# Kernel optimization log

Hardware: AMD Instinct MI355X
Metric: run time of the kernel (lower is better)

Reference implementation:

```python
import jax, jax.numpy as jnp
import numpy as np
from math import factorial

N_NODES = 50000
N_EDGES = 500000
NUM_BASIS = 10
HIDDEN = 64
MUL_OUT = 8  # irreps_out_per_basis = '8x0e + 8x1o + 8x2e'

# ---------- real Wigner-3j (Clebsch-Gordan in real SH basis) ----------

def _cg(j1, m1, j2, m2, j3, m3):
    # complex Clebsch-Gordan <j1 m1 j2 m2 | j3 m3> (Racah formula)
    if m1 + m2 != m3:
        return 0.0
    f = factorial
    pre = ((2*j3+1) * f(j1+j2-j3) * f(j1-j2+j3) * f(-j1+j2+j3) / f(j1+j2+j3+1)) ** 0.5
    pre *= (f(j1+m1)*f(j1-m1)*f(j2+m2)*f(j2-m2)*f(j3+m3)*f(j3-m3)) ** 0.5
    s = 0.0
    for k in range(max(0, j2-j3-m1, j1-j3+m2), min(j1+j2-j3, j1-m1, j2+m2) + 1):
        s += (-1)**k / (f(k)*f(j1+j2-j3-k)*f(j1-m1-k)*f(j2+m2-k)*f(j3-j2+m1+k)*f(j3-j1-m2+k))
    return pre * s

def _q(l):
    # complex -> real spherical-harmonic change of basis, m ordered -l..l
    Q = np.zeros((2*l+1, 2*l+1), dtype=complex)
    Q[l, l] = 1.0
    for m in range(1, l+1):
        Q[l+m, l+m] = (-1)**m / np.sqrt(2.0); Q[l+m, l-m] = 1.0/np.sqrt(2.0)
        Q[l-m, l-m] = 1j / np.sqrt(2.0);      Q[l-m, l+m] = -1j*(-1)**m/np.sqrt(2.0)
    return Q

def _w3j(l1, l2, l3):
    C = np.zeros((2*l1+1, 2*l2+1, 2*l3+1), dtype=complex)
    for a, m1 in enumerate(range(-l1, l1+1)):
        for b, m2 in enumerate(range(-l2, l2+1)):
            for c, m3 in enumerate(range(-l3, l3+1)):
                C[a, b, c] = _cg(l1, m1, l2, m2, l3, m3)
    R = np.einsum('ab,cd,ef,bdf->ace', _q(l1).conj(), _q(l2).conj(), _q(l3), C)
    if np.abs(R.imag).max() > np.abs(R.real).max():
        R = -1j * R
    R = np.real(R)
    return (R / np.linalg.norm(R)).astype(np.float32)

# allowed (l2, l3) paths for each input block l1 (parity-filtered to 0e/1o/2e output)
PATHS = {0: [(0, 0), (1, 1), (2, 2)],
         1: [(0, 1), (1, 0), (1, 2), (2, 1)],
         2: [(0, 2), (1, 1), (2, 0), (2, 2)]}
MUL1 = {0: 1, 1: 3, 2: 5}
W3J = {(l1, l2, l3): jnp.asarray(_w3j(l1, l2, l3))
       for l1, ps in PATHS.items() for (l2, l3) in ps}
FAN = {l1: {l3: sum(MUL1[l1] for (_, l3b) in PATHS[l1] if l3b == l3) for l3 in (0, 1, 2)}
       for l1 in (0, 1, 2)}
WNUMEL = {l1: len(PATHS[l1]) * MUL1[l1] * MUL_OUT for l1 in (0, 1, 2)}  # 24, 96, 160

# ---------- forward pieces ----------

def _sh(unit):
    # component-normalized real spherical harmonics, lmax=2, e3nn (y,z,x) order for l=1
    x, y, z = unit[:, 0], unit[:, 1], unit[:, 2]
    sh0 = jnp.ones_like(x)[:, None]
    sh1 = jnp.sqrt(3.0) * jnp.stack([y, z, x], axis=1)
    sh2 = jnp.stack([jnp.sqrt(15.0)*x*y, jnp.sqrt(15.0)*y*z,
                     jnp.sqrt(5.0)/2.0*(3.0*z*z - 1.0), jnp.sqrt(15.0)*x*z,
                     jnp.sqrt(15.0)/2.0*(x*x - y*y)], axis=1)
    return {0: sh0, 1: sh1, 2: sh2}

def _soft_one_hot(d, max_radius):
    # e3nn soft_one_hot_linspace, basis='smooth_finite', cutoff=True
    values = jnp.linspace(0.0, float(max_radius), NUM_BASIS + 2)[1:-1]
    step = float(max_radius) / (NUM_BASIS + 1)
    diff = (d[:, None] - values) / step
    def sus(t):
        return jnp.where(t > 0.0, jnp.exp(-1.0 / jnp.where(t > 0.0, t, 1.0)), 0.0)
    e = 1.14136 * np.exp(2.0) * sus(diff + 1.0) * sus(1.0 - diff)
    return e * np.sqrt(float(NUM_BASIS))

def _fc(x, w1, w2):
    # e3nn FullyConnectedNet: variance-preserving linear + normalized relu
    h = (x @ w1) / np.sqrt(float(w1.shape[0]))
    h = jax.nn.relu(h) * np.sqrt(2.0)
    return (h @ w2) / np.sqrt(float(w2.shape[0]))

def _tp(l1, x1, shs, w_flat):
    # FullyConnectedTensorProduct (uvw, shared_weights=False, component/element norm)
    # x1: [E, mul1, 2l1+1], w_flat: [E, WNUMEL[l1]]
    E = x1.shape[0]
    outs = {l3: jnp.zeros((E, MUL_OUT, 2*l3+1), x1.dtype) for l3 in (0, 1, 2)}
    off = 0
    for (l2, l3) in PATHS[l1]:
        n = MUL1[l1] * MUL_OUT
        w = w_flat[:, off:off+n].reshape(E, MUL1[l1], MUL_OUT)
        off += n
        pw = np.sqrt((2*l3 + 1) / float(FAN[l1][l3]))
        outs[l3] = outs[l3] + pw * jnp.einsum('eui,ej,ijk,euw->ewk',
                                              x1, shs[l2], W3J[(l1, l2, l3)], w)
    return jnp.concatenate([outs[l3].reshape(E, -1) for l3 in (0, 1, 2)], axis=1)

def _forward(x, edge_index, pos, max_radius, num_nodes, ws1, ws2, wp1, wp2, wd1, wd2):
    row, col = edge_index[0], edge_index[1]
    edge_vec = pos[row] - pos[col]                          # [E,3]
    d = jnp.sqrt(jnp.sum(edge_vec * edge_vec, axis=1) + 1e-12)
    shs = _sh(edge_vec / d[:, None])
    emb = _soft_one_hot(d, max_radius)                      # [E,NUM_BASIS]
    w_s = _fc(emb, ws1, ws2)
    w_p = _fc(emb, wp1, wp2)
    w_d = _fc(emb, wd1, wd2)
    f = x.reshape(-1, 9, 9, 2)
    fsum = f[..., 0] + f[..., 1]  # TP is linear in input 1: tp(a,w)+tp(b,w)=tp(a+b,w)
    out_s = _tp(0, fsum[:, 0:1, 0:1].reshape(-1, 1, 1)[row], shs, w_s)
    out_p = _tp(1, fsum[:, 1:4, 1:4].reshape(-1, 3, 3)[row], shs, w_p)
    out_d = _tp(2, fsum[:, 4:9, 4:9].reshape(-1, 5, 5)[row], shs, w_d)
    summand = jnp.concatenate([out_s, out_p, out_d], axis=1)  # [E,216]
    f_out = jax.ops.segment_sum(summand, col, num_segments=num_nodes)
    return f_out / np.sqrt(edge_index.shape[1] / float(num_nodes))


def setup_inputs() -> dict:
    key = jax.random.key(0)
    ks = jax.random.split(key, 10)
    x = jax.random.normal(ks[0], (N_NODES, 162), jnp.float32)
    pos = jax.random.normal(ks[1], (N_NODES, 3), jnp.float32) * 2.0
    row = jax.random.randint(ks[2], (N_EDGES,), 0, N_NODES)
    col = (row + jax.random.randint(ks[3], (N_EDGES,), 1, N_NODES)) % N_NODES  # no self-loops
    edge_index = jnp.stack([row, col]).astype(jnp.int32)
    return {
        'x': x, 'edge_index': edge_index, 'pos': pos,
        'max_radius': 5, 'num_nodes': N_NODES,
        'fc_s_w1': jax.random.normal(ks[4], (NUM_BASIS, HIDDEN), jnp.float32),
        'fc_s_w2': jax.random.normal(ks[5], (HIDDEN, WNUMEL[0]), jnp.float32),
        'fc_p_w1': jax.random.normal(ks[6], (NUM_BASIS, HIDDEN), jnp.float32),
        'fc_p_w2': jax.random.normal(ks[7], (HIDDEN, WNUMEL[1]), jnp.float32),
        'fc_d_w1': jax.random.normal(ks[8], (NUM_BASIS, HIDDEN), jnp.float32),
        'fc_d_w2': jax.random.normal(ks[9], (HIDDEN, WNUMEL[2]), jnp.float32),
    }


def reference(x, edge_index, pos, max_radius, num_nodes,
              fc_s_w1, fc_s_w2, fc_p_w1, fc_p_w2, fc_d_w1, fc_d_w2):
    return _forward(x, edge_index, pos, max_radius, num_nodes,
                    fc_s_w1, fc_s_w2, fc_p_w1, fc_p_w2, fc_d_w1, fc_d_w2)
```

## Files before the change

### kernel.cpp

```cpp
#include <hip/hip_runtime.h>

#define BLK 128
#define RSTR 76
#define W1OFF (35*512)

__device__ __forceinline__ double dfac(int n){
  const double T[8] = {1.0,1.0,2.0,6.0,24.0,120.0,720.0,5040.0};
  return T[n];
}

__device__ __forceinline__ double cgc(int j1,int m1,int j2,int m2,int j3,int m3){
  if (m1+m2 != m3) return 0.0;
  double pre = sqrt((double)(2*j3+1) * dfac(j1+j2-j3)*dfac(j1-j2+j3)*dfac(-j1+j2+j3)/dfac(j1+j2+j3+1));
  pre *= sqrt(dfac(j1+m1)*dfac(j1-m1)*dfac(j2+m2)*dfac(j2-m2)*dfac(j3+m3)*dfac(j3-m3));
  int kmin = 0; if (j2-j3-m1 > kmin) kmin = j2-j3-m1; if (j1-j3+m2 > kmin) kmin = j1-j3+m2;
  int kmax = j1+j2-j3; if (j1-m1 < kmax) kmax = j1-m1; if (j2+m2 < kmax) kmax = j2+m2;
  double s = 0.0;
  for (int k=kmin;k<=kmax;++k){
    double t = 1.0/(dfac(k)*dfac(j1+j2-j3-k)*dfac(j1-m1-k)*dfac(j2+m2-k)*dfac(j3-j2+m1+k)*dfac(j3-j1-m2+k));
    s += (k&1)? -t : t;
  }
  return pre*s;
}

__device__ __forceinline__ void qval(int l, int a, int b, double& qr, double& qi){
  qr = 0.0; qi = 0.0;
  int ma = a - l, mb = b - l;
  if (ma==0){ if (mb==0) qr = 1.0; return; }
  const double is2 = 0.7071067811865476;
  if (ma > 0){
    if (mb == ma)       qr = (ma&1)? -is2 : is2;
    else if (mb == -ma) qr = is2;
  } else {
    int m = -ma;
    if (mb == ma)       qi = is2;
    else if (mb == m)   qi = (m&1)? is2 : -is2;
  }
}

__global__ __launch_bounds__(384) void w3j_kernel(float* __restrict__ w3j){
  __shared__ double Rr[363], Ri[363];
  __shared__ double sInv[11];
  __shared__ int    sFlip[11];
  const int L1t[11] = {0,0,0,1,1,1,1,2,2,2,2};
  const int L2t[11] = {0,1,2,0,1,1,2,0,1,2,2};
  const int L3t[11] = {0,1,2,1,0,2,1,2,1,0,2};
  const int OFFt[12]= {0,1,10,35,44,53,98,143,168,213,238,363};

  int g = threadIdx.x;
  bool act = g < 363;
  int t = 0, l1=0, l2=0, l3=0;
  if (act){
    while (g >= OFFt[t+1]) t++;
    l1=L1t[t]; l2=L2t[t]; l3=L3t[t];
    int n2=2*l2+1, n3=2*l3+1;
    int local = g - OFFt[t];
    int e  = local % n3;
    int tm = local / n3;
    int c  = tm % n2;
    int a  = tm / n2;
    double sr=0.0, si=0.0;
    for (int b=0; b<2*l1+1; b++){
      double q1r,q1i; qval(l1,a,b,q1r,q1i); q1i = -q1i;
      if (q1r==0.0 && q1i==0.0) continue;
      for (int dd=0; dd<n2; dd++){
        double q2r,q2i; qval(l2,c,dd,q2r,q2i); q2i = -q2i;
        if (q2r==0.0 && q2i==0.0) continue;
        double pr = q1r*q2r - q1i*q2i;
        double pi = q1r*q2i + q1i*q2r;
        for (int f=0; f<n3; f++){
          double cg = cgc(l1,b-l1,l2,dd-l2,l3,f-l3);
          if (cg==0.0) continue;
          double q3r,q3i; qval(l3,e,f,q3r,q3i);
          sr += cg*(pr*q3r - pi*q3i);
          si += cg*(pr*q3i + pi*q3r);
        }
      }
    }
    Rr[g]=sr; Ri[g]=si;
  }
  __syncthreads();
  if (threadIdx.x < 11){
    int tt = threadIdx.x;
    int lo = OFFt[tt], hi = OFFt[tt+1];
    double mxr=0.0, mxi=0.0;
    for (int i=lo;i<hi;i++){
      double ar=fabs(Rr[i]), ai=fabs(Ri[i]);
      if (ar>mxr) mxr=ar;
      if (ai>mxi) mxi=ai;
    }
    int flip = (mxi > mxr) ? 1 : 0;
    double nrm=0.0;
    for (int i=lo;i<hi;i++){ double v = flip? Ri[i] : Rr[i]; nrm += v*v; }
    sInv[tt]  = 1.0/sqrt(nrm);
    sFlip[tt] = flip;
  }
  __syncthreads();
  if (act){
    double v = sFlip[t] ? Ri[g] : Rr[g];
    w3j[g] = (float)(v * sInv[t]);
  }
}

__global__ void pack_kernel(const float* __restrict__ x, float* __restrict__ xp, int tot){
  int i = blockIdx.x*256 + threadIdx.x;
  if (i >= tot) return;
  int n = i/35, j = i - n*35;
  int src;
  if (j == 0)       src = 0;
  else if (j < 10){ int r=j-1;  src = (1 + r/3)*9 + 1 + r%3; }
  else            { int r=j-10; src = (4 + r/5)*9 + 4 + r%5; }
  const float* b = x + (size_t)n*162 + src*2;
  xp[i] = b[0] + b[1];
}

__global__ void repack_kernel(const float* __restrict__ w2s, const float* __restrict__ w2p,
                              const float* __restrict__ w2d,
                              const float* __restrict__ w1s, const float* __restrict__ w1p,
                              const float* __restrict__ w1d, float* __restrict__ wr){
  int i = blockIdx.x*256 + threadIdx.x;
  int tot2 = 35*512;
  if (i < tot2){
    int blk = i >> 9;
    int idx = i & 511;
    int hc = idx >> 3, w = idx & 7;
    const float* src; int WN, cb, u;
    if (blk < 3){ src=w2s; WN=24; cb=blk*8; u=0; }
    else if (blk < 15){ int b=blk-3; int p=b/3; u=b-p*3; src=w2p; WN=96; const int cbs[4]={0,24,48,72}; cb=cbs[p]; }
    else { int b=blk-15; int p=b/5; u=b-p*5; src=w2d; WN=160; const int cbs[4]={0,40,80,120}; cb=cbs[p]; }
    wr[i] = src[hc*WN + cb + u*8 + w];
  } else if (i < tot2 + 3*640){
    int r = i - tot2;
    int c = r/640; int rem = r - c*640;
    int chunk = rem/40; int idx = rem - chunk*40;
    int b = idx>>2, j = idx&3;
    const float* src = (c==0)? w1s : (c==1)? w1p : w1d;
    wr[i] = src[b*64 + chunk*4 + j];
  }
}

__device__ __forceinline__ bool edge_ok(const float* __restrict__ pos, int row, int col, float mrf){
  float ax = pos[3*row+0]-pos[3*col+0];
  float ay = pos[3*row+1]-pos[3*col+1];
  float az = pos[3*row+2]-pos[3*col+2];
  float d  = sqrtf(fmaf(ax,ax, fmaf(ay,ay, fmaf(az,az, 1e-12f))));
  return d < mrf;
}

__global__ void hist_kernel(const int* __restrict__ ei, const float* __restrict__ pos,
                            const int* __restrict__ mrp, int* __restrict__ cnt, int E){
  int e = blockIdx.x*256 + threadIdx.x;
  if (e >= E) return;
  int row = ei[e], col = ei[E+e];
  if (edge_ok(pos,row,col,(float)mrp[0])) atomicAdd(&cnt[col], 1);
}

__device__ __forceinline__ int wscan(int v, int lane){
  #pragma unroll
  for (int s=1;s<64;s<<=1){
    int t = __shfl_up(v, s);
    if (lane >= s) v += t;
  }
  return v;
}

__global__ void scan_kernel(int* __restrict__ cnt, int* __restrict__ off, int N){
  __shared__ int wsum[16];
  __shared__ int srun;
  int t=threadIdx.x, lane=t&63, w=t>>6;
  if (t==0) srun=0;
  __syncthreads();
  for (int base=0; base<N; base+=1024){
    int v = (base+t<N) ? cnt[base+t] : 0;
    int incl = wscan(v, lane);
    if (lane==63) wsum[w]=incl;
    __syncthreads();
    int run = srun;
    int woff = 0;
    for (int i=0;i<w;i++) woff += wsum[i];
    int ex = run + woff + incl - v;
    if (base+t<N){ off[base+t]=ex; cnt[base+t]=ex; }
    __syncthreads();
    if (t==1023) srun = run + woff + incl;
    __syncthreads();
  }
  if (t==0) off[N]=srun;
}

__global__ void scatter_kernel(const int* __restrict__ ei, const float* __restrict__ pos,
                               const int* __restrict__ mrp, int* __restrict__ cursor,
                               int* __restrict__ csrR, int* __restrict__ csrC, int E){
  int e = blockIdx.x*256 + threadIdx.x;
  if (e >= E) return;
  int row = ei[e], col = ei[E+e];
  if (edge_ok(pos,row,col,(float)mrp[0])){
    int s = atomicAdd(&cursor[col], 1);
    csrR[s] = row;
    csrC[s] = col;
  }
}

__device__ __forceinline__ void compute_h(const float (&emb)[10], const float* __restrict__ w1r, float* hrow){
  const float RS10 = 0.31622776601683794f;
  #pragma unroll 2
  for (int i=0; i<16; ++i){
    const float* r = w1r + i*40;
    float a0=0.f,a1=0.f,a2=0.f,a3=0.f;
    #pragma unroll
    for (int b=0;b<10;b++){
      a0 = fmaf(emb[b], r[b*4+0], a0);
      a1 = fmaf(emb[b], r[b*4+1], a1);
      a2 = fmaf(emb[b], r[b*4+2], a2);
      a3 = fmaf(emb[b], r[b*4+3], a3);
    }
    float4 hv;
    hv.x = fmaxf(a0*RS10, 0.f);
    hv.y = fmaxf(a1*RS10, 0.f);
    hv.z = fmaxf(a2*RS10, 0.f);
    hv.w = fmaxf(a3*RS10, 0.f);
    *reinterpret_cast<float4*>(hrow+i*4) = hv;
  }
}

__device__ __forceinline__ void compute_h_raw(const float (&emb)[10], const float* __restrict__ w1, float* hrow){
  const float RS10 = 0.31622776601683794f;
  #pragma unroll 1
  for (int hh=0; hh<64; hh+=4){
    float a0=0.f,a1=0.f,a2=0.f,a3=0.f;
    #pragma unroll
    for (int b=0;b<10;b++){
      const float* r = w1 + b*64 + hh;
      a0 = fmaf(emb[b], r[0], a0);
      a1 = fmaf(emb[b], r[1], a1);
      a2 = fmaf(emb[b], r[2], a2);
      a3 = fmaf(emb[b], r[3], a3);
    }
    float4 hv;
    hv.x = fmaxf(a0*RS10, 0.f);
    hv.y = fmaxf(a1*RS10, 0.f);
    hv.z = fmaxf(a2*RS10, 0.f);
    hv.w = fmaxf(a3*RS10, 0.f);
    *reinterpret_cast<float4*>(hrow+hh) = hv;
  }
}

template<int L1, int L2, int L3, int W3JOFF>
__device__ __forceinline__ void calc_s(const float* __restrict__ w3j,
    const float (&x1)[2*L1+1], const float (&sh1)[3], const float (&sh2)[5],
    float CP, float (&s)[2*L3+1])
{
  constexpr int N1=2*L1+1, N2=2*L2+1, N3=2*L3+1;
  #pragma unroll
  for (int k=0;k<N3;k++) s[k]=0.f;
  #pragma unroll
  for (int i=0;i<N1;i++){
    #pragma unroll
    for (int j=0;j<N2;j++){
      float shv = (L2==0) ? 1.0f : ((L2==1) ? sh1[j] : sh2[j]);
      float c = x1[i]*shv;
      #pragma unroll
      for (int k=0;k<N3;k++)
        s[k] = fmaf(c, w3j[W3JOFF + (i*N2+j)*N3 + k], s[k]);
    }
  }
  #pragma unroll
  for (int k=0;k<N3;k++) s[k] *= CP;
}

template<int P>
__device__ __forceinline__ void wg_pass_r(const float* __restrict__ wr,
    const int (&blks)[P], const float* __restrict__ hrow, float (&wg)[P][8])
{
  #pragma unroll
  for (int p=0;p<P;p++)
    #pragma unroll
    for (int w=0;w<8;w++) wg[p][w]=0.f;
  #pragma unroll 4
  for (int hc=0;hc<64;hc+=4){
    float4 hv = *reinterpret_cast<const float4*>(hrow+hc);
    #pragma unroll
    for (int p=0;p<P;p++){
      const float* r0 = wr + blks[p]*512 + hc*8;
      #pragma unroll
      for (int w=0;w<8;w++){
        float t0 = fmaf(hv.x, r0[w],    wg[p][w]);
        t0       = fmaf(hv.y, r0[8+w],  t0);
        t0       = fmaf(hv.z, r0[16+w], t0);
        wg[p][w] = fmaf(hv.w, r0[24+w], t0);
      }
    }
  }
}

template<int P, int WN>
__device__ __forceinline__ void wg_pass(const float* __restrict__ w2,
    const int (&cb)[P], int u8, const float* __restrict__ hrow, float (&wg)[P][8])
{
  #pragma unroll
  for (int p=0;p<P;p++)
    #pragma unroll
    for (int w=0;w<8;w++) wg[p][w]=0.f;
  #pragma unroll 1
  for (int hc=0;hc<64;hc+=4){
    float4 hv = *reinterpret_cast<const float4*>(hrow+hc);
    #pragma unroll
    for (int p=0;p<P;p++){
      const float* r0 = w2 + cb[p] + u8 + hc*WN;
      #pragma unroll
      for (int w=0;w<8;w++){
        float t0 = fmaf(hv.x, r0[w],      wg[p][w]);
        t0       = fmaf(hv.y, r0[WN+w],   t0);
        t0       = fmaf(hv.z, r0[2*WN+w], t0);
        wg[p][w] = fmaf(hv.w, r0[3*WN+w], t0);
      }
    }
  }
}

template<int N3, int OUTB>
__device__ __forceinline__ void acc_o(const float (&wgp)[8], const float (&s)[N3], float (&o)[72]){
  #pragma unroll
  for (int w=0;w<8;w++){
    #pragma unroll
    for (int k=0;k<N3;k++)
      o[OUTB + w*N3 + k] = fmaf(wgp[w], s[k], o[OUTB + w*N3 + k]);
  }
}

template<bool PACKED>
__global__ __launch_bounds__(BLK) void edge_kernel_csr(
  const int* __restrict__ csrR, const int* __restrict__ csrC,
  const int* __restrict__ off, int N,
  const float* __restrict__ pos, const float* __restrict__ x, const float* __restrict__ xp,
  const float* __restrict__ w3j, const int* __restrict__ mrp,
  const float* __restrict__ wr,
  float* __restrict__ out, float rs)
{
  __shared__ __align__(16) float hb[BLK*RSTR];
  __shared__ int scol[BLK];
  __shared__ int lmeta[BLK];
  __shared__ int lcount;

  int tid = threadIdx.x;
  int blockBase = blockIdx.x*BLK;
  int Ev = off[N];
  if (blockBase >= Ev) return;
  int slot = blockBase + tid;
  bool valid = slot < Ev;
  int row = valid ? csrR[slot] : 0;
  int key = valid ? csrC[slot] : -1;
  int colIdx = valid ? key : 0;

  scol[tid] = key;
  if (tid==0) lcount = 0;
  __syncthreads();
  if (valid && (tid==0 || scol[tid-1]!=key)){
    int len=1;
    while (tid+len<BLK && scol[tid+len]==key) len++;
    int comp = (off[key] >= blockBase) && (off[key+1] <= blockBase+BLK);
    int idx = atomicAdd(&lcount, 1);
    lmeta[idx] = tid | (len<<8) | (comp<<31);
  }
  __syncthreads();
  int lc = lcount;

  float ax = pos[3*row+0]-pos[3*colIdx+0];
  float ay = pos[3*row+1]-pos[3*colIdx+1];
  float az = pos[3*row+2]-pos[3*colIdx+2];
  float d  = sqrtf(fmaf(ax,ax, fmaf(ay,ay, fmaf(az,az, 1e-12f))));
  float mrf = (float)mrp[0];
  float inv = 1.0f/d;
  float ux=ax*inv, uy=ay*inv, uz=az*inv;
  float sh1[3] = {1.7320508075688772f*uy, 1.7320508075688772f*uz, 1.7320508075688772f*ux};
  float sh2[5] = {3.872983346207417f*ux*uy, 3.872983346207417f*uy*uz,
                  1.118033988749895f*(3.f*uz*uz-1.f), 3.872983346207417f*ux*uz,
                  1.9364916731037085f*(ux*ux-uy*uy)};
  float emb[10];
  {
    float xs = d * (11.0f/mrf);
    float CE = 1.14136f * expf(2.0f) * sqrtf(10.0f);
    #pragma unroll
    for (int b=0;b<10;b++){
      float t1 = xs - (float)b;
      float t2 = (float)(b+2) - xs;
      float s1 = (t1>0.f)? expf(-1.0f/t1) : 0.f;
      float s2 = (t2>0.f)? expf(-1.0f/t2) : 0.f;
      emb[b] = CE*s1*s2;
    }
  }

  float* hrow = &hb[tid*RSTR];
  const float* xrow = PACKED ? (xp + (size_t)row*35) : (x + (size_t)row*162);
  const float* w1r = wr + W1OFF;

  auto flush_reduce = [&](const float (&o)[72], int PO){
    #pragma unroll
    for (int i=0;i<72;i+=4){
      float4 v; v.x=o[i]; v.y=o[i+1]; v.z=o[i+2]; v.w=o[i+3];
      *reinterpret_cast<float4*>(hrow+i) = v;
    }
    __syncthreads();
    int total = lc*72;
    for (int task = tid; task < total; task += BLK){
      int li = task/72;
      int el = task - li*72;
      int meta = lmeta[li];
      int s0  = meta & 255;
      int len = (meta>>8) & 255;
      int c   = scol[s0];
      float sum = 0.f;
      const float* p = &hb[s0*RSTR + el];
      for (int i=0;i<len;i++) sum += p[i*RSTR];
      float* dst = out + (size_t)c*216 + PO + el;
      if (meta < 0) *dst = sum;
      else unsafeAtomicAdd(dst, sum);
    }
    __syncthreads();
  };

  {
    compute_h(emb, w1r + 0, hrow);
    float o[72];
    #pragma unroll
    for (int i=0;i<72;i++) o[i]=0.f;
    float x1[1];
    x1[0] = PACKED ? xrow[0] : (xrow[0]+xrow[1]);
    float sA[1], sB[3], sC[5];
    calc_s<0,0,0,  0>(w3j,x1,sh1,sh2, 0.17677669529663687f*rs, sA);
    calc_s<0,1,1,  1>(w3j,x1,sh1,sh2, 0.30618621784789724f*rs, sB);
    calc_s<0,2,2, 10>(w3j,x1,sh1,sh2, 0.39528470752104744f*rs, sC);
    float wg[3][8];
    const int blks[3] = {0,1,2};
    wg_pass_r<3>(wr, blks, hrow, wg);
    acc_o<1, 0>(wg[0], sA, o);
    acc_o<3, 8>(wg[1], sB, o);
    acc_o<5,32>(wg[2], sC, o);
    flush_reduce(o, 0);
  }
  {
    compute_h(emb, w1r + 640, hrow);
    float o[72];
    #pragma unroll
    for (int i=0;i<72;i++) o[i]=0.f;
    #pragma unroll 1
    for (int u=0;u<3;++u){
      float x1[3];
      #pragma unroll
      for (int i=0;i<3;i++){
        int src = ((1+u)*9 + 1+i)*2;
        x1[i] = PACKED ? xrow[1+u*3+i] : (xrow[src]+xrow[src+1]);
      }
      float sA[3], sB[1], sC[5], sD[3];
      calc_s<1,0,1, 35>(w3j,x1,sh1,sh2, 0.125f*rs,               sA);
      calc_s<1,1,0, 44>(w3j,x1,sh1,sh2, 0.10206207261596577f*rs, sB);
      calc_s<1,1,2, 53>(w3j,x1,sh1,sh2, 0.22821773229381923f*rs, sC);
      calc_s<1,2,1, 98>(w3j,x1,sh1,sh2, 0.125f*rs,               sD);
      float wg[4][8];
      const int blks[4] = {3+u, 6+u, 9+u, 12+u};
      wg_pass_r<4>(wr, blks, hrow, wg);
      acc_o<3, 8>(wg[0], sA, o);
      acc_o<1, 0>(wg[1], sB, o);
      acc_o<5,32>(wg[2], sC, o);
      acc_o<3, 8>(wg[3], sD, o);
    }
    flush_reduce(o, 72);
  }
  {
    compute_h(emb, w1r + 1280, hrow);
    float o[72];
    #pragma unroll
    for (int i=0;i<72;i++) o[i]=0.f;
    #pragma unroll 1
    for (int u=0;u<5;++u){
      float x1[5];
      #pragma unroll
      for (int i=0;i<5;i++){
        int src = ((4+u)*9 + 4+i)*2;
        x1[i] = PACKED ? xrow[10+u*5+i] : (xrow[src]+xrow[src+1]);
      }
      float sA[5], sB[3], sC[1], sD[5];
      calc_s<2,0,2,143>(w3j,x1,sh1,sh2, 0.125f*rs,               sA);
      calc_s<2,1,1,168>(w3j,x1,sh1,sh2, 0.13693063937629152f*rs, sB);
      calc_s<2,2,0,213>(w3j,x1,sh1,sh2, 0.07905694150420948f*rs, sC);
      calc_s<2,2,2,238>(w3j,x1,sh1,sh2, 0.125f*rs,               sD);
      float wg[4][8];
      const int blks[4] = {15+u, 20+u, 25+u, 30+u};
      wg_pass_r<4>(wr, blks, hrow, wg);
      acc_o<5,32>(wg[0], sA, o);
      acc_o<3, 8>(wg[1], sB, o);
      acc_o<1, 0>(wg[2], sC, o);
      acc_o<5,32>(wg[3], sD, o);
    }
    flush_reduce(o, 144);
  }
}

__device__ __forceinline__ void flush72(const float (&o)[72], float* dst){
  #pragma unroll
  for (int i=0;i<72;i++) unsafeAtomicAdd(dst+i, o[i]);
}

__global__ __launch_bounds__(BLK) void edge_kernel_atomic(
  const int* __restrict__ ei, const float* __restrict__ pos,
  const float* __restrict__ x,
  const float* __restrict__ w3j, const int* __restrict__ mrp,
  const float* __restrict__ w1s, const float* __restrict__ w2s,
  const float* __restrict__ w1p, const float* __restrict__ w2p,
  const float* __restrict__ w1d, const float* __restrict__ w2d,
  float* __restrict__ out, int E, float rs)
{
  __shared__ __align__(16) float hbA[BLK*RSTR];
  int e = blockIdx.x*BLK + threadIdx.x;
  if (e >= E) return;
  int row = ei[e], col = ei[E+e];
  float ax = pos[3*row+0]-pos[3*col+0];
  float ay = pos[3*row+1]-pos[3*col+1];
  float az = pos[3*row+2]-pos[3*col+2];
  float d  = sqrtf(fmaf(ax,ax, fmaf(ay,ay, fmaf(az,az, 1e-12f))));
  float mrf = (float)mrp[0];
  if (d >= mrf) return;
  float inv = 1.0f/d;
  float ux=ax*inv, uy=ay*inv, uz=az*inv;
  float sh1[3] = {1.7320508075688772f*uy, 1.7320508075688772f*uz, 1.7320508075688772f*ux};
  float sh2[5] = {3.872983346207417f*ux*uy, 3.872983346207417f*uy*uz,
                  1.118033988749895f*(3.f*uz*uz-1.f), 3.872983346207417f*ux*uz,
                  1.9364916731037085f*(ux*ux-uy*uy)};
  float emb[10];
  {
    float xs = d * (11.0f/mrf);
    float CE = 1.14136f * expf(2.0f) * sqrtf(10.0f);
    #pragma unroll
    for (int b=0;b<10;b++){
      float t1 = xs - (float)b;
      float t2 = (float)(b+2) - xs;
      float s1 = (t1>0.f)? expf(-1.0f/t1) : 0.f;
      float s2 = (t2>0.f)? expf(-1.0f/t2) : 0.f;
      emb[b] = CE*s1*s2;
    }
  }
  float* hrow = &hbA[threadIdx.x*RSTR];
  const float* xrow = x + (size_t)row*162;
  float* obase = out + (size_t)col*216;
  {
    compute_h_raw(emb, w1s, hrow);
    float o[72];
    #pragma unroll
    for (int i=0;i<72;i++) o[i]=0.f;
    float x1[1] = { xrow[0]+xrow[1] };
    float sA[1], sB[3], sC[5];
    calc_s<0,0,0,  0>(w3j,x1,sh1,sh2, 0.17677669529663687f*rs, sA);
    calc_s<0,1,1,  1>(w3j,x1,sh1,sh2, 0.30618621784789724f*rs, sB);
    calc_s<0,2,2, 10>(w3j,x1,sh1,sh2, 0.39528470752104744f*rs, sC);
    float wg[3][8];
    const int cb[3] = {0,8,16};
    wg_pass<3,24>(w2s, cb, 0, hrow, wg);
    acc_o<1, 0>(wg[0], sA, o);
    acc_o<3, 8>(wg[1], sB, o);
    acc_o<5,32>(wg[2], sC, o);
    flush72(o, obase);
  }
  {
    compute_h_raw(emb, w1p, hrow);
    float o[72];
    #pragma unroll
    for (int i=0;i<72;i++) o[i]=0.f;
    #pragma unroll 1
    for (int u=0;u<3;++u){
      float x1[3];
      #pragma unroll
      for (int i=0;i<3;i++){ int src = ((1+u)*9 + 1+i)*2; x1[i] = xrow[src]+xrow[src+1]; }
      float sA[3], sB[1], sC[5], sD[3];
      calc_s<1,0,1, 35>(w3j,x1,sh1,sh2, 0.125f*rs,               sA);
      calc_s<1,1,0, 44>(w3j,x1,sh1,sh2, 0.10206207261596577f*rs, sB);
      calc_s<1,1,2, 53>(w3j,x1,sh1,sh2, 0.22821773229381923f*rs, sC);
      calc_s<1,2,1, 98>(w3j,x1,sh1,sh2, 0.125f*rs,               sD);
      float wg[4][8];
      const int cb[4] = {0,24,48,72};
      wg_pass<4,96>(w2p, cb, u*8, hrow, wg);
      acc_o<3, 8>(wg[0], sA, o);
      acc_o<1, 0>(wg[1], sB, o);
      acc_o<5,32>(wg[2], sC, o);
      acc_o<3, 8>(wg[3], sD, o);
    }
    flush72(o, obase + 72);
  }
  {
    compute_h_raw(emb, w1d, hrow);
    float o[72];
    #pragma unroll
    for (int i=0;i<72;i++) o[i]=0.f;
    #pragma unroll 1
    for (int u=0;u<5;++u){
      float x1[5];
      #pragma unroll
      for (int i=0;i<5;i++){ int src = ((4+u)*9 + 4+i)*2; x1[i] = xrow[src]+xrow[src+1]; }
      float sA[5], sB[3], sC[1], sD[5];
      calc_s<2,0,2,143>(w3j,x1,sh1,sh2, 0.125f*rs,               sA);
      calc_s<2,1,1,168>(w3j,x1,sh1,sh2, 0.13693063937629152f*rs, sB);
      calc_s<2,2,0,213>(w3j,x1,sh1,sh2, 0.07905694150420948f*rs, sC);
      calc_s<2,2,2,238>(w3j,x1,sh1,sh2, 0.125f*rs,               sD);
      float wg[4][8];
      const int cb[4] = {0,40,80,120};
      wg_pass<4,160>(w2d, cb, u*8, hrow, wg);
      acc_o<5,32>(wg[0], sA, o);
      acc_o<3, 8>(wg[1], sB, o);
      acc_o<1, 0>(wg[2], sC, o);
      acc_o<5,32>(wg[3], sD, o);
    }
    flush72(o, obase + 144);
  }
}

extern "C" void kernel_launch(void* const* d_in, const int* in_sizes, int n_in,
                              void* d_out, int out_size, void* d_ws, size_t ws_size,
                              hipStream_t stream){
  (void)n_in; (void)out_size;
  const float* x   = (const float*)d_in[0];
  const int*   ei  = (const int*)  d_in[1];
  const float* pos = (const float*)d_in[2];
  const int*   mr  = (const int*)  d_in[3];
  const float* w1s = (const float*)d_in[5];
  const float* w2s = (const float*)d_in[6];
  const float* w1p = (const float*)d_in[7];
  const float* w2p = (const float*)d_in[8];
  const float* w1d = (const float*)d_in[9];
  const float* w2d = (const float*)d_in[10];

  int N = in_sizes[0]/162;
  int E = in_sizes[1]/2;
  float rs = sqrtf((float)N/(float)E);

  auto alignup = [](size_t v){ return (v + 255) & ~(size_t)255; };
  size_t o_off  = 0;
  size_t o_cnt  = alignup(o_off + (size_t)(N+1)*4);
  size_t o_csrR = alignup(o_cnt + (size_t)N*4);
  size_t o_csrC = alignup(o_csrR + (size_t)E*4);
  size_t o_w3j  = alignup(o_csrC + (size_t)E*4);
  size_t o_wr   = alignup(o_w3j + 2048);
  size_t o_xp   = alignup(o_wr + (size_t)(35*512 + 3*640)*4);
  size_t needB  = o_xp;
  size_t needA  = o_xp + (size_t)N*35*4;

  char* wsb = (char*)d_ws;
  hipMemsetAsync(d_out, 0, (size_t)N*216*sizeof(float), stream);

  if (ws_size >= needB){
    int*   off  = (int*)(wsb + o_off);
    int*   cnt  = (int*)(wsb + o_cnt);
    int*   csrR = (int*)(wsb + o_csrR);
    int*   csrC = (int*)(wsb + o_csrC);
    float* w3j  = (float*)(wsb + o_w3j);
    float* wr   = (float*)(wsb + o_wr);
    float* xp   = (float*)(wsb + o_xp);

    hipMemsetAsync(cnt, 0, (size_t)N*4, stream);
    w3j_kernel<<<1,384,0,stream>>>(w3j);
    int rtot = 35*512 + 3*640;
    repack_kernel<<<(rtot+255)/256,256,0,stream>>>(w2s, w2p, w2d, w1s, w1p, w1d, wr);
    hist_kernel<<<(E+255)/256,256,0,stream>>>(ei, pos, mr, cnt, E);
    scan_kernel<<<1,1024,0,stream>>>(cnt, off, N);
    scatter_kernel<<<(E+255)/256,256,0,stream>>>(ei, pos, mr, cnt, csrR, csrC, E);

    int nblk = (E + BLK - 1)/BLK;
    if (ws_size >= needA){
      int tot = N*35;
      pack_kernel<<<(tot+255)/256,256,0,stream>>>(x, xp, tot);
      edge_kernel_csr<true><<<nblk, BLK, 0, stream>>>(
        csrR, csrC, off, N, pos, x, xp, w3j, mr, wr, (float*)d_out, rs);
    } else {
      edge_kernel_csr<false><<<nblk, BLK, 0, stream>>>(
        csrR, csrC, off, N, pos, x, x, w3j, mr, wr, (float*)d_out, rs);
    }
  } else {
    float* w3j = (float*)wsb;
    w3j_kernel<<<1,384,0,stream>>>(w3j);
    edge_kernel_atomic<<<(E+BLK-1)/BLK, BLK, 0, stream>>>(
      ei, pos, x, w3j, mr, w1s, w2s, w1p, w2p, w1d, w2d, (float*)d_out, E, rs);
  }
}
```

Before: 624.7 us.

## Stage tensor-product weights and Wigner-3j tables in shared memory per block

Reorders the repacked second-layer weights so the four path blocks used together for each input multiplicity sit next to each other. The CSR edge kernel then copies the weights, first-layer weights and w3j coefficients into LDS, with extra barriers between stages. This is meant to replace uniform global/L1 loads in the inner weight GEMV with broadcast LDS reads. The cost is about 12 KB more shared memory per block, which may lower occupancy, plus added __syncthreads and the staging copies themselves. The inner loop unroll also drops to 1.

```diff
diff --git a/kernel.cpp b/kernel.cpp
--- a/kernel.cpp
+++ b/kernel.cpp
@@ -126,8 +126,8 @@
     int hc = idx >> 3, w = idx & 7;
     const float* src; int WN, cb, u;
     if (blk < 3){ src=w2s; WN=24; cb=blk*8; u=0; }
-    else if (blk < 15){ int b=blk-3; int p=b/3; u=b-p*3; src=w2p; WN=96; const int cbs[4]={0,24,48,72}; cb=cbs[p]; }
-    else { int b=blk-15; int p=b/5; u=b-p*5; src=w2d; WN=160; const int cbs[4]={0,40,80,120}; cb=cbs[p]; }
+    else if (blk < 15){ int b=blk-3; u=b>>2; int p=b&3; src=w2p; WN=96; const int cbs[4]={0,24,48,72}; cb=cbs[p]; }
+    else { int b=blk-15; u=b>>2; int p=b&3; src=w2d; WN=160; const int cbs[4]={0,40,80,120}; cb=cbs[p]; }
     wr[i] = src[hc*WN + cb + u*8 + w];
   } else if (i < tot2 + 3*640){
     int r = i - tot2;
@@ -268,19 +268,19 @@
 }
 
 template<int P>
-__device__ __forceinline__ void wg_pass_r(const float* __restrict__ wr,
-    const int (&blks)[P], const float* __restrict__ hrow, float (&wg)[P][8])
+__device__ __forceinline__ void wg_pass_l(const float* __restrict__ wb,
+    const float* __restrict__ hrow, float (&wg)[P][8])
 {
   #pragma unroll
   for (int p=0;p<P;p++)
     #pragma unroll
     for (int w=0;w<8;w++) wg[p][w]=0.f;
-  #pragma unroll 4
+  #pragma unroll 1
   for (int hc=0;hc<64;hc+=4){
     float4 hv = *reinterpret_cast<const float4*>(hrow+hc);
     #pragma unroll
     for (int p=0;p<P;p++){
-      const float* r0 = wr + blks[p]*512 + hc*8;
+      const float* r0 = wb + p*512 + hc*8;
       #pragma unroll
       for (int w=0;w<8;w++){
         float t0 = fmaf(hv.x, r0[w],    wg[p][w]);
@@ -337,6 +337,9 @@
   float* __restrict__ out, float rs)
 {
   __shared__ __align__(16) float hb[BLK*RSTR];
+  __shared__ __align__(16) float wbuf[2048];
+  __shared__ __align__(16) float w1b[640];
+  __shared__ __align__(16) float w3jb[368];
   __shared__ int scol[BLK];
   __shared__ int lmeta[BLK];
   __shared__ int lcount;
@@ -351,8 +354,14 @@
   int key = valid ? csrC[slot] : -1;
   int colIdx = valid ? key : 0;
 
+  auto stage = [&](const float* __restrict__ src, float* __restrict__ dst, int nf){
+    for (int i = tid*4; i < nf; i += BLK*4)
+      *reinterpret_cast<float4*>(dst + i) = *reinterpret_cast<const float4*>(src + i);
+  };
+
   scol[tid] = key;
   if (tid==0) lcount = 0;
+  stage(w3j, w3jb, 368);
   __syncthreads();
   if (valid && (tid==0 || scol[tid-1]!=key)){
     int len=1;
@@ -361,6 +370,8 @@
     int idx = atomicAdd(&lcount, 1);
     lmeta[idx] = tid | (len<<8) | (comp<<31);
   }
+  stage(wr, wbuf, 1536);
+  stage(wr + W1OFF, w1b, 640);
   __syncthreads();
   int lc = lcount;
 
@@ -391,7 +402,6 @@
 
   float* hrow = &hb[tid*RSTR];
   const float* xrow = PACKED ? (xp + (size_t)row*35) : (x + (size_t)row*162);
-  const float* w1r = wr + W1OFF;
 
   auto flush_reduce = [&](const float (&o)[72], int PO){
     #pragma unroll
@@ -419,31 +429,38 @@
   };
 
   {
-    compute_h(emb, w1r + 0, hrow);
+    compute_h(emb, w1b, hrow);
     float o[72];
     #pragma unroll
     for (int i=0;i<72;i++) o[i]=0.f;
     float x1[1];
     x1[0] = PACKED ? xrow[0] : (xrow[0]+xrow[1]);
     float sA[1], sB[3], sC[5];
-    calc_s<0,0,0,  0>(w3j,x1,sh1,sh2, 0.17677669529663687f*rs, sA);
-    calc_s<0,1,1,  1>(w3j,x1,sh1,sh2, 0.30618621784789724f*rs, sB);
-    calc_s<0,2,2, 10>(w3j,x1,sh1,sh2, 0.39528470752104744f*rs, sC);
+    calc_s<0,0,0,  0>(w3jb,x1,sh1,sh2, 0.17677669529663687f*rs, sA);
+    calc_s<0,1,1,  1>(w3jb,x1,sh1,sh2, 0.30618621784789724f*rs, sB);
+    calc_s<0,2,2, 10>(w3jb,x1,sh1,sh2, 0.39528470752104744f*rs, sC);
     float wg[3][8];
-    const int blks[3] = {0,1,2};
-    wg_pass_r<3>(wr, blks, hrow, wg);
+    wg_pass_l<3>(wbuf, hrow, wg);
     acc_o<1, 0>(wg[0], sA, o);
     acc_o<3, 8>(wg[1], sB, o);
     acc_o<5,32>(wg[2], sC, o);
     flush_reduce(o, 0);
   }
   {
-    compute_h(emb, w1r + 640, hrow);
+    stage(wr + W1OFF + 640, w1b, 640);
+    stage(wr + 3*512, wbuf, 2048);
+    __syncthreads();
+    compute_h(emb, w1b, hrow);
     float o[72];
     #pragma unroll
     for (int i=0;i<72;i++) o[i]=0.f;
     #pragma unroll 1
     for (int u=0;u<3;++u){
+      if (u > 0){
+        __syncthreads();
+        stage(wr + (3+u*4)*512, wbuf, 2048);
+        __syncthreads();
+      }
       float x1[3];
       #pragma unroll
       for (int i=0;i<3;i++){
@@ -451,13 +468,12 @@
         x1[i] = PACKED ? xrow[1+u*3+i] : (xrow[src]+xrow[src+1]);
       }
       float sA[3], sB[1], sC[5], sD[3];
-      calc_s<1,0,1, 35>(w3j,x1,sh1,sh2, 0.125f*rs,               sA);
-      calc_s<1,1,0, 44>(w3j,x1,sh1,sh2, 0.10206207261596577f*rs, sB);
-      calc_s<1,1,2, 53>(w3j,x1,sh1,sh2, 0.22821773229381923f*rs, sC);
-      calc_s<1,2,1, 98>(w3j,x1,sh1,sh2, 0.125f*rs,               sD);
+      calc_s<1,0,1, 35>(w3jb,x1,sh1,sh2, 0.125f*rs,               sA);
+      calc_s<1,1,0, 44>(w3jb,x1,sh1,sh2, 0.10206207261596577f*rs, sB);
+      calc_s<1,1,2, 53>(w3jb,x1,sh1,sh2, 0.22821773229381923f*rs, sC);
+      calc_s<1,2,1, 98>(w3jb,x1,sh1,sh2, 0.125f*rs,               sD);
       float wg[4][8];
-      const int blks[4] = {3+u, 6+u, 9+u, 12+u};
-      wg_pass_r<4>(wr, blks, hrow, wg);
+      wg_pass_l<4>(wbuf, hrow, wg);
       acc_o<3, 8>(wg[0], sA, o);
       acc_o<1, 0>(wg[1], sB, o);
       acc_o<5,32>(wg[2], sC, o);
@@ -466,12 +482,20 @@
     flush_reduce(o, 72);
   }
   {
-    compute_h(emb, w1r + 1280, hrow);
+    stage(wr + W1OFF + 1280, w1b, 640);
+    stage(wr + 15*512, wbuf, 2048);
+    __syncthreads();
+    compute_h(emb, w1b, hrow);
     float o[72];
     #pragma unroll
     for (int i=0;i<72;i++) o[i]=0.f;
     #pragma unroll 1
     for (int u=0;u<5;++u){
+      if (u > 0){
+        __syncthreads();
+        stage(wr + (15+u*4)*512, wbuf, 2048);
+        __syncthreads();
+      }
       float x1[5];
       #pragma unroll
       for (int i=0;i<5;i++){
@@ -479,13 +503,12 @@
         x1[i] = PACKED ? xrow[10+u*5+i] : (xrow[src]+xrow[src+1]);
       }
       float sA[5], sB[3], sC[1], sD[5];
-      calc_s<2,0,2,143>(w3j,x1,sh1,sh2, 0.125f*rs,               sA);
-      calc_s<2,1,1,168>(w3j,x1,sh1,sh2, 0.13693063937629152f*rs, sB);
-      calc_s<2,2,0,213>(w3j,x1,sh1,sh2, 0.07905694150420948f*rs, sC);
-      calc_s<2,2,2,238>(w3j,x1,sh1,sh2, 0.125f*rs,               sD);
+      calc_s<2,0,2,143>(w3jb,x1,sh1,sh2, 0.125f*rs,               sA);
+      calc_s<2,1,1,168>(w3jb,x1,sh1,sh2, 0.13693063937629152f*rs, sB);
+      calc_s<2,2,0,213>(w3jb,x1,sh1,sh2, 0.07905694150420948f*rs, sC);
+      calc_s<2,2,2,238>(w3jb,x1,sh1,sh2, 0.125f*rs,               sD);
       float wg[4][8];
-      const int blks[4] = {15+u, 20+u, 25+u, 30+u};
-      wg_pass_r<4>(wr, blks, hrow, wg);
+      wg_pass_l<4>(wbuf, hrow, wg);
       acc_o<5,32>(wg[0], sA, o);
       acc_o<3, 8>(wg[1], sB, o);
       acc_o<1, 0>(wg[2], sC, o);
```

New measurement: 701.9 us. +12.4%, slower.
